# Kernel optimization log

Hardware: AMD Instinct MI355X
Metric: run time of the kernel (lower is better)

## Reference

```python
import jax, jax.numpy as jnp
import numpy as np

N_NODES = 8192   # = in_feats (module ties n_nodes to linear width)
D_FEAT = 512
N_EDGES = 262144  # avg degree 32


def setup_inputs() -> dict:
    key = jax.random.key(0)
    k1, k2, k3 = jax.random.split(key, 3)
    x = jax.random.normal(k1, (D_FEAT, N_NODES), dtype=jnp.float32)
    adj = jax.random.randint(k2, (2, N_EDGES), 0, N_NODES, dtype=jnp.int32)
    # nn.Linear(in_feats, in_feats, bias=False) weight, kaiming-ish scale
    W = jax.random.normal(k3, (N_NODES, N_NODES), dtype=jnp.float32) * (1.0 / np.sqrt(N_NODES))
    return {"x": x, "adj": adj, "W": W}


def reference(x, adj, W):
    # x: [D, N]; adj: [2, E] (row, col); W: [N, N]
    row, col = adj[0], adj[1]
    n = x.shape[1]
    # deg = bincount(row, minlength=N).clamp(min=1)
    deg = jax.ops.segment_sum(jnp.ones_like(row, dtype=x.dtype), row, num_segments=n)
    deg = jnp.maximum(deg, 1.0)
    # spmm(A, ones, N, N, x.T): agg[r] += x.T[c] for each edge (r, c) -> [N, D]
    agg = jax.ops.segment_sum(x.T[col], row, num_segments=n)
    h = agg.T / deg  # [D, N], divide each column by its degree
    # F.relu(self.lin(h)) with Linear applied on last dim (size N = in_feats)
    return jax.nn.relu(h @ W.T)
```

## Files before the change

### kernel.cpp

```cpp
#include <hip/hip_runtime.h>
#include <hip/hip_bf16.h>
#include <stdint.h>

#define NN 8192
#define DD 512
#define EE 262144

typedef __attribute__((ext_vector_type(8))) short short8;
typedef __attribute__((ext_vector_type(4))) float f32x4;

__device__ __forceinline__ unsigned short f2bf_rne(float f) {
    unsigned u = __float_as_uint(f);
    u += 0x7fffu + ((u >> 16) & 1u);
    return (unsigned short)(u >> 16);
}

__device__ __forceinline__ void gload_lds16(const void* g, void* l) {
    __builtin_amdgcn_global_load_lds(
        (const __attribute__((address_space(1))) unsigned int*)g,
        (__attribute__((address_space(3))) unsigned int*)l, 16, 0, 0);
}

__global__ void k_init(int* deg, int* cursor) {
    int i = blockIdx.x * 256 + threadIdx.x;
    if (i < NN) { deg[i] = 0; cursor[i] = 0; }
}

__global__ void k_hist(const int* __restrict__ row, int* __restrict__ deg) {
    int e = blockIdx.x * 256 + threadIdx.x;
    if (e < EE) atomicAdd(&deg[row[e]], 1);
}

__global__ void k_scan(const int* __restrict__ deg, int* __restrict__ offsets,
                       int* __restrict__ cursor) {
    __shared__ int psum[256];
    int t = threadIdx.x;
    int base = t * 32;
    int local[32];
    int s = 0;
    for (int i = 0; i < 32; i++) { local[i] = s; s += deg[base + i]; }
    psum[t] = s;
    __syncthreads();
    int pre = 0;
    for (int i = 0; i < t; i++) pre += psum[i];
    for (int i = 0; i < 32; i++) {
        int v = pre + local[i];
        offsets[base + i] = v;
        cursor[base + i] = v;
    }
    if (t == 255) offsets[NN] = pre + s;
}

__global__ void k_scatter(const int* __restrict__ row, const int* __restrict__ col,
                          int* __restrict__ cursor, int* __restrict__ csr) {
    int e = blockIdx.x * 256 + threadIdx.x;
    if (e < EE) {
        int r = row[e];
        int p = atomicAdd(&cursor[r], 1);
        csr[p] = col[e];
    }
}

__global__ void k_xt(const float* __restrict__ x, unsigned short* __restrict__ xTb) {
    __shared__ float tile[32][33];
    int tx = threadIdx.x & 31, ty = threadIdx.x >> 5;
    int n0 = blockIdx.x * 32;
    int d0 = blockIdx.y * 32;
    #pragma unroll
    for (int i = 0; i < 32; i += 8)
        tile[ty + i][tx] = x[(size_t)(d0 + ty + i) * NN + n0 + tx];
    __syncthreads();
    #pragma unroll
    for (int i = 0; i < 32; i += 8)
        xTb[(size_t)(n0 + ty + i) * DD + d0 + tx] = f2bf_rne(tile[tx][ty + i]);
}

__global__ void k_agg(const unsigned short* __restrict__ xTb, const int* __restrict__ offsets,
                      const int* __restrict__ csr, unsigned short* __restrict__ hTb) {
    __shared__ int nb[128];
    int r = blockIdx.x;
    int t = threadIdx.x;
    int s = offsets[r], e = offsets[r + 1];
    int d = e - s;
    float inv = 1.0f / (float)(d > 0 ? d : 1);
    float a0 = 0.f, a1 = 0.f, a2 = 0.f, a3 = 0.f;
    for (int base = s; base < e; base += 128) {
        int cnt = min(128, e - base);
        if (t < cnt) nb[t] = csr[base + t];
        __syncthreads();
        for (int j = 0; j < cnt; j++) {
            int c = nb[j];
            uint2 u = *(const uint2*)(xTb + (size_t)c * DD + t * 4);
            a0 += __uint_as_float(u.x << 16);
            a1 += __uint_as_float(u.x & 0xffff0000u);
            a2 += __uint_as_float(u.y << 16);
            a3 += __uint_as_float(u.y & 0xffff0000u);
        }
        __syncthreads();
    }
    unsigned short o0 = f2bf_rne(a0 * inv), o1 = f2bf_rne(a1 * inv);
    unsigned short o2 = f2bf_rne(a2 * inv), o3 = f2bf_rne(a3 * inv);
    ushort4 o = make_ushort4(o0, o1, o2, o3);
    *(ushort4*)(hTb + (size_t)r * DD + t * 4) = o;
}

__global__ void k_ht(const unsigned short* __restrict__ hTb, unsigned short* __restrict__ hA) {
    __shared__ unsigned short tile[32][33];
    int tx = threadIdx.x & 31, ty = threadIdx.x >> 5;
    int r0 = blockIdx.x * 32;
    int d0 = blockIdx.y * 32;
    #pragma unroll
    for (int i = 0; i < 32; i += 8)
        tile[ty + i][tx] = hTb[(size_t)(r0 + ty + i) * DD + d0 + tx];
    __syncthreads();
    #pragma unroll
    for (int i = 0; i < 32; i += 8)
        hA[(size_t)(d0 + ty + i) * NN + r0 + tx] = tile[tx][ty + i];
}

__global__ void k_zero(float4* part) {
    int i = blockIdx.x * 256 + threadIdx.x;
    part[i] = make_float4(0.f, 0.f, 0.f, 0.f);
}

__global__ __launch_bounds__(256, 2)
void k_gemm(const unsigned short* __restrict__ hA, const float* __restrict__ W,
            float* __restrict__ part) {
    __shared__ unsigned short As[128 * 64];
    __shared__ unsigned short Bs[128 * 72];

    const int bid = blockIdx.x;
    const int g = (bid & 7) | ((bid >> 5) << 3);
    const int mt = (bid >> 3) & 3;
    const int nt = g >> 1;
    const int ks = g & 1;
    const int m0 = mt * 128, n0 = nt * 128;
    const int kbeg = ks * 4096, kend = kbeg + 4096;

    const int tid = threadIdx.x;
    const int lane = tid & 63, wave = tid >> 6;
    const int wm = (wave & 1) * 64, wn = (wave >> 1) * 64;
    const int l15 = lane & 15, quad = lane >> 4;

    f32x4 acc[4][4];
    #pragma unroll
    for (int i = 0; i < 4; i++)
        #pragma unroll
        for (int j = 0; j < 4; j++) acc[i][j] = (f32x4){0.f, 0.f, 0.f, 0.f};

    const int arow = tid >> 3;
    const int acol_log = ((tid & 7) ^ (arow & 7)) * 8;
    const int aphys = (tid & 7) * 8;

    for (int k0 = kbeg; k0 < kend; k0 += 64) {
        __syncthreads();
        #pragma unroll
        for (int i = 0; i < 4; i++) {
            int r = arow + i * 32;
            gload_lds16(hA + (size_t)(m0 + r) * NN + k0 + acol_log, &As[r * 64 + aphys]);
        }
        float4 wv[8];
        #pragma unroll
        for (int i = 0; i < 8; i++) {
            int fid = tid + i * 256;
            int rw = fid >> 4, c4 = fid & 15;
            wv[i] = *(const float4*)(W + (size_t)(n0 + rw) * NN + k0 + c4 * 4);
        }
        #pragma unroll
        for (int i = 0; i < 8; i++) {
            int fid = tid + i * 256;
            int rw = fid >> 4, c4 = fid & 15;
            unsigned p0 = __builtin_amdgcn_perm(__float_as_uint(wv[i].y) + 0x8000u,
                                                __float_as_uint(wv[i].x) + 0x8000u, 0x07060302u);
            unsigned p1 = __builtin_amdgcn_perm(__float_as_uint(wv[i].w) + 0x8000u,
                                                __float_as_uint(wv[i].z) + 0x8000u, 0x07060302u);
            *(uint2*)&Bs[rw * 72 + c4 * 4] = make_uint2(p0, p1);
        }
        __syncthreads();
        #pragma unroll
        for (int kk = 0; kk < 64; kk += 32) {
            short8 af[4], bf[4];
            #pragma unroll
            for (int mi = 0; mi < 4; mi++) {
                int row = wm + mi * 16 + l15;
                int pc = (((kk >> 3) + quad) ^ (l15 & 7)) * 8;
                af[mi] = *(const short8*)&As[row * 64 + pc];
            }
            #pragma unroll
            for (int ni = 0; ni < 4; ni++)
                bf[ni] = *(const short8*)&Bs[(wn + ni * 16 + l15) * 72 + kk + quad * 8];
            #pragma unroll
            for (int mi = 0; mi < 4; mi++)
                #pragma unroll
                for (int ni = 0; ni < 4; ni++)
                    acc[mi][ni] = __builtin_amdgcn_mfma_f32_16x16x32_bf16(
                        af[mi], bf[ni], acc[mi][ni], 0, 0, 0);
        }
    }
    #pragma unroll
    for (int mi = 0; mi < 4; mi++)
        #pragma unroll
        for (int ni = 0; ni < 4; ni++) {
            int mrow = m0 + wm + mi * 16 + quad * 4;
            int ncol = n0 + wn + ni * 16 + l15;
            #pragma unroll
            for (int i = 0; i < 4; i++)
                atomicAdd(&part[(size_t)(mrow + i) * NN + ncol], acc[mi][ni][i]);
        }
}

__global__ void k_relu(float4* __restrict__ buf) {
    int i = blockIdx.x * 256 + threadIdx.x;
    float4 v = buf[i];
    buf[i] = make_float4(fmaxf(v.x, 0.f), fmaxf(v.y, 0.f), fmaxf(v.z, 0.f), fmaxf(v.w, 0.f));
}

extern "C" void kernel_launch(void* const* d_in, const int* in_sizes, int n_in,
                              void* d_out, int out_size, void* d_ws, size_t ws_size,
                              hipStream_t stream) {
    const float* x = (const float*)d_in[0];
    const int* adj = (const int*)d_in[1];
    const float* W = (const float*)d_in[2];
    char* ws = (char*)d_ws;

    const int* row = adj;
    const int* col = adj + EE;

    int* deg = (int*)(ws + 0);
    int* cursor = (int*)(ws + 32768);
    int* offsets = (int*)(ws + 65536);
    int* csr = (int*)(ws + 131072);
    unsigned short* xTb = (unsigned short*)(ws + (2u << 20));
    unsigned short* hA = xTb;
    unsigned short* hTb = (unsigned short*)d_out;
    float* part = (float*)d_out;

    k_init<<<32, 256, 0, stream>>>(deg, cursor);
    k_hist<<<EE / 256, 256, 0, stream>>>(row, deg);
    k_scan<<<1, 256, 0, stream>>>(deg, offsets, cursor);
    k_scatter<<<EE / 256, 256, 0, stream>>>(row, col, cursor, csr);
    k_xt<<<dim3(NN / 32, DD / 32), 256, 0, stream>>>(x, xTb);
    k_agg<<<NN, 128, 0, stream>>>(xTb, offsets, csr, hTb);
    k_ht<<<dim3(NN / 32, DD / 32), 256, 0, stream>>>(hTb, hA);
    k_zero<<<4096, 256, 0, stream>>>((float4*)part);
    k_gemm<<<512, 256, 0, stream>>>(hA, W, part);
    k_relu<<<4096, 256, 0, stream>>>((float4*)part);
}
```

Baseline: 523.4 us.

## Drop LDS staging in GEMM; load MFMA fragments directly with register double-buffering

The GEMM kernel no longer stages A and W tiles through shared memory with barriers. Each wave now loads its MFMA operand fragments straight from global memory into registers, using two register buffers so the next k-step's loads are in flight while the current MFMA batch runs. W is converted to bf16 in registers just before use. This removes LDS traffic and __syncthreads stalls, but loses data reuse across waves: each A and W row is fetched by two waves, and the direct global access pattern is less coalesced, with more register pressure.

```diff
diff --git a/kernel.cpp b/kernel.cpp
--- a/kernel.cpp
+++ b/kernel.cpp
@@ -13,12 +13,6 @@
     unsigned u = __float_as_uint(f);
     u += 0x7fffu + ((u >> 16) & 1u);
     return (unsigned short)(u >> 16);
-}
-
-__device__ __forceinline__ void gload_lds16(const void* g, void* l) {
-    __builtin_amdgcn_global_load_lds(
-        (const __attribute__((address_space(1))) unsigned int*)g,
-        (__attribute__((address_space(3))) unsigned int*)l, 16, 0, 0);
 }
 
 __global__ void k_init(int* deg, int* cursor) {
@@ -123,15 +117,55 @@
     part[i] = make_float4(0.f, 0.f, 0.f, 0.f);
 }
 
+struct afrag { short8 v[4]; };
+struct wfrag { float4 v[4][2]; };
+
+__device__ __forceinline__ void load_a(afrag& f, const unsigned short* aptr, int k) {
+    #pragma unroll
+    for (int mi = 0; mi < 4; mi++)
+        f.v[mi] = *(const short8*)(aptr + (size_t)mi * 16 * NN + k);
+}
+__device__ __forceinline__ void load_w(wfrag& f, const float* wptr, int k) {
+    #pragma unroll
+    for (int ni = 0; ni < 4; ni++) {
+        f.v[ni][0] = *(const float4*)(wptr + (size_t)ni * 16 * NN + k);
+        f.v[ni][1] = *(const float4*)(wptr + (size_t)ni * 16 * NN + k + 4);
+    }
+}
+__device__ __forceinline__ short8 pack_bf16(const float4& a, const float4& b) {
+    unsigned p0 = __builtin_amdgcn_perm(__float_as_uint(a.y) + 0x8000u,
+                                        __float_as_uint(a.x) + 0x8000u, 0x07060302u);
+    unsigned p1 = __builtin_amdgcn_perm(__float_as_uint(a.w) + 0x8000u,
+                                        __float_as_uint(a.z) + 0x8000u, 0x07060302u);
+    unsigned p2 = __builtin_amdgcn_perm(__float_as_uint(b.y) + 0x8000u,
+                                        __float_as_uint(b.x) + 0x8000u, 0x07060302u);
+    unsigned p3 = __builtin_amdgcn_perm(__float_as_uint(b.w) + 0x8000u,
+                                        __float_as_uint(b.z) + 0x8000u, 0x07060302u);
+    union { unsigned u[4]; short8 s; } r;
+    r.u[0] = p0; r.u[1] = p1; r.u[2] = p2; r.u[3] = p3;
+    return r.s;
+}
+__device__ __forceinline__ void compute(f32x4 acc[4][4], const afrag& a, const wfrag& w) {
+    short8 bf[4];
+    #pragma unroll
+    for (int ni = 0; ni < 4; ni++) bf[ni] = pack_bf16(w.v[ni][0], w.v[ni][1]);
+    #pragma unroll
+    for (int mi = 0; mi < 4; mi++)
+        #pragma unroll
+        for (int ni = 0; ni < 4; ni++)
+            acc[mi][ni] = __builtin_amdgcn_mfma_f32_16x16x32_bf16(
+                a.v[mi], bf[ni], acc[mi][ni], 0, 0, 0);
+}
+
 __global__ __launch_bounds__(256, 2)
 void k_gemm(const unsigned short* __restrict__ hA, const float* __restrict__ W,
             float* __restrict__ part) {
-    __shared__ unsigned short As[128 * 64];
-    __shared__ unsigned short Bs[128 * 72];
-
     const int bid = blockIdx.x;
-    const int g = (bid & 7) | ((bid >> 5) << 3);
-    const int mt = (bid >> 3) & 3;
+    const int x = bid & 7;
+    const int l = bid >> 3;
+    const int mt = l & 3;
+    const int ghi = l >> 2;
+    const int g = ghi * 8 + x;
     const int nt = g >> 1;
     const int ks = g & 1;
     const int m0 = mt * 128, n0 = nt * 128;
@@ -142,61 +176,29 @@
     const int wm = (wave & 1) * 64, wn = (wave >> 1) * 64;
     const int l15 = lane & 15, quad = lane >> 4;
 
+    const unsigned short* aptr = hA + (size_t)(m0 + wm + l15) * NN + quad * 8;
+    const float* wptr = W + (size_t)(n0 + wn + l15) * NN + quad * 8;
+
     f32x4 acc[4][4];
     #pragma unroll
     for (int i = 0; i < 4; i++)
         #pragma unroll
         for (int j = 0; j < 4; j++) acc[i][j] = (f32x4){0.f, 0.f, 0.f, 0.f};
 
-    const int arow = tid >> 3;
-    const int acol_log = ((tid & 7) ^ (arow & 7)) * 8;
-    const int aphys = (tid & 7) * 8;
+    afrag aA, aB;
+    wfrag wA, wB;
+    load_a(aA, aptr, kbeg);      load_w(wA, wptr, kbeg);
+    load_a(aB, aptr, kbeg + 32); load_w(wB, wptr, kbeg + 32);
 
     for (int k0 = kbeg; k0 < kend; k0 += 64) {
-        __syncthreads();
-        #pragma unroll
-        for (int i = 0; i < 4; i++) {
-            int r = arow + i * 32;
-            gload_lds16(hA + (size_t)(m0 + r) * NN + k0 + acol_log, &As[r * 64 + aphys]);
-        }
-        float4 wv[8];
-        #pragma unroll
-        for (int i = 0; i < 8; i++) {
-            int fid = tid + i * 256;
-            int rw = fid >> 4, c4 = fid & 15;
-            wv[i] = *(const float4*)(W + (size_t)(n0 + rw) * NN + k0 + c4 * 4);
-        }
-        #pragma unroll
-        for (int i = 0; i < 8; i++) {
-            int fid = tid + i * 256;
-            int rw = fid >> 4, c4 = fid & 15;
-            unsigned p0 = __builtin_amdgcn_perm(__float_as_uint(wv[i].y) + 0x8000u,
-                                                __float_as_uint(wv[i].x) + 0x8000u, 0x07060302u);
-            unsigned p1 = __builtin_amdgcn_perm(__float_as_uint(wv[i].w) + 0x8000u,
-                                                __float_as_uint(wv[i].z) + 0x8000u, 0x07060302u);
-            *(uint2*)&Bs[rw * 72 + c4 * 4] = make_uint2(p0, p1);
-        }
-        __syncthreads();
-        #pragma unroll
-        for (int kk = 0; kk < 64; kk += 32) {
-            short8 af[4], bf[4];
-            #pragma unroll
-            for (int mi = 0; mi < 4; mi++) {
-                int row = wm + mi * 16 + l15;
-                int pc = (((kk >> 3) + quad) ^ (l15 & 7)) * 8;
-                af[mi] = *(const short8*)&As[row * 64 + pc];
-            }
-            #pragma unroll
-            for (int ni = 0; ni < 4; ni++)
-                bf[ni] = *(const short8*)&Bs[(wn + ni * 16 + l15) * 72 + kk + quad * 8];
-            #pragma unroll
-            for (int mi = 0; mi < 4; mi++)
-                #pragma unroll
-                for (int ni = 0; ni < 4; ni++)
-                    acc[mi][ni] = __builtin_amdgcn_mfma_f32_16x16x32_bf16(
-                        af[mi], bf[ni], acc[mi][ni], 0, 0, 0);
-        }
-    }
+        int kpA = (k0 + 64 < kend) ? k0 + 64 : kbeg;
+        int kpB = (k0 + 96 < kend) ? k0 + 96 : kbeg;
+        compute(acc, aA, wA);
+        load_a(aA, aptr, kpA); load_w(wA, wptr, kpA);
+        compute(acc, aB, wB);
+        load_a(aB, aptr, kpB); load_w(wB, wptr, kpB);
+    }
+
     #pragma unroll
     for (int mi = 0; mi < 4; mi++)
         #pragma unroll
```

Measured after the change: 895.4 us. +71.1%, slower.

## Double-buffer GEMM LDS tiles to overlap next-tile loads with MFMA

Applied to the files above, without the earlier changes.

Splits the A and B shared-memory tiles into two buffers and prefetches the next K-slice while MFMAs run on the current one. W is loaded into registers before compute and converted to bf16 into the other buffer afterwards, and A goes straight to LDS asynchronously. This hides global load latency behind compute and removes one barrier per iteration. In exchange it doubles LDS use, to about 68KB per block, which could limit the two-blocks-per-CU occupancy target, and it holds the prefetched W values in registers across the MFMA section.

```diff
diff --git a/kernel.cpp b/kernel.cpp
--- a/kernel.cpp
+++ b/kernel.cpp
@@ -126,8 +126,8 @@
 __global__ __launch_bounds__(256, 2)
 void k_gemm(const unsigned short* __restrict__ hA, const float* __restrict__ W,
             float* __restrict__ part) {
-    __shared__ unsigned short As[128 * 64];
-    __shared__ unsigned short Bs[128 * 72];
+    __shared__ unsigned short As[2][128 * 64];
+    __shared__ unsigned short Bs[2][128 * 72];
 
     const int bid = blockIdx.x;
     const int g = (bid & 7) | ((bid >> 5) << 3);
@@ -151,32 +151,45 @@
     const int arow = tid >> 3;
     const int acol_log = ((tid & 7) ^ (arow & 7)) * 8;
     const int aphys = (tid & 7) * 8;
-
+    const int brow = tid >> 4;
+    const int bc4 = tid & 15;
+
+    float4 wv[8];
+
+    #pragma unroll
+    for (int i = 0; i < 8; i++)
+        wv[i] = *(const float4*)(W + (size_t)(n0 + brow + i * 16) * NN + kbeg + bc4 * 4);
+    #pragma unroll
+    for (int i = 0; i < 4; i++) {
+        int r = arow + i * 32;
+        gload_lds16(hA + (size_t)(m0 + r) * NN + kbeg + acol_log, &As[0][r * 64 + aphys]);
+    }
+    #pragma unroll
+    for (int i = 0; i < 8; i++) {
+        unsigned p0 = __builtin_amdgcn_perm(__float_as_uint(wv[i].y) + 0x8000u,
+                                            __float_as_uint(wv[i].x) + 0x8000u, 0x07060302u);
+        unsigned p1 = __builtin_amdgcn_perm(__float_as_uint(wv[i].w) + 0x8000u,
+                                            __float_as_uint(wv[i].z) + 0x8000u, 0x07060302u);
+        *(uint2*)&Bs[0][(brow + i * 16) * 72 + bc4 * 4] = make_uint2(p0, p1);
+    }
+    __syncthreads();
+
+    int cur = 0;
     for (int k0 = kbeg; k0 < kend; k0 += 64) {
-        __syncthreads();
-        #pragma unroll
-        for (int i = 0; i < 4; i++) {
-            int r = arow + i * 32;
-            gload_lds16(hA + (size_t)(m0 + r) * NN + k0 + acol_log, &As[r * 64 + aphys]);
-        }
-        float4 wv[8];
-        #pragma unroll
-        for (int i = 0; i < 8; i++) {
-            int fid = tid + i * 256;
-            int rw = fid >> 4, c4 = fid & 15;
-            wv[i] = *(const float4*)(W + (size_t)(n0 + rw) * NN + k0 + c4 * 4);
-        }
-        #pragma unroll
-        for (int i = 0; i < 8; i++) {
-            int fid = tid + i * 256;
-            int rw = fid >> 4, c4 = fid & 15;
-            unsigned p0 = __builtin_amdgcn_perm(__float_as_uint(wv[i].y) + 0x8000u,
-                                                __float_as_uint(wv[i].x) + 0x8000u, 0x07060302u);
-            unsigned p1 = __builtin_amdgcn_perm(__float_as_uint(wv[i].w) + 0x8000u,
-                                                __float_as_uint(wv[i].z) + 0x8000u, 0x07060302u);
-            *(uint2*)&Bs[rw * 72 + c4 * 4] = make_uint2(p0, p1);
-        }
-        __syncthreads();
+        const bool has_next = (k0 + 64 < kend);
+        if (has_next) {
+            #pragma unroll
+            for (int i = 0; i < 8; i++)
+                wv[i] = *(const float4*)(W + (size_t)(n0 + brow + i * 16) * NN +
+                                         (k0 + 64) + bc4 * 4);
+            #pragma unroll
+            for (int i = 0; i < 4; i++) {
+                int r = arow + i * 32;
+                gload_lds16(hA + (size_t)(m0 + r) * NN + (k0 + 64) + acol_log,
+                            &As[cur ^ 1][r * 64 + aphys]);
+            }
+            __builtin_amdgcn_sched_barrier(0);
+        }
         #pragma unroll
         for (int kk = 0; kk < 64; kk += 32) {
             short8 af[4], bf[4];
@@ -184,11 +197,11 @@
             for (int mi = 0; mi < 4; mi++) {
                 int row = wm + mi * 16 + l15;
                 int pc = (((kk >> 3) + quad) ^ (l15 & 7)) * 8;
-                af[mi] = *(const short8*)&As[row * 64 + pc];
+                af[mi] = *(const short8*)&As[cur][row * 64 + pc];
             }
             #pragma unroll
             for (int ni = 0; ni < 4; ni++)
-                bf[ni] = *(const short8*)&Bs[(wn + ni * 16 + l15) * 72 + kk + quad * 8];
+                bf[ni] = *(const short8*)&Bs[cur][(wn + ni * 16 + l15) * 72 + kk + quad * 8];
             #pragma unroll
             for (int mi = 0; mi < 4; mi++)
                 #pragma unroll
@@ -196,7 +209,20 @@
                     acc[mi][ni] = __builtin_amdgcn_mfma_f32_16x16x32_bf16(
                         af[mi], bf[ni], acc[mi][ni], 0, 0, 0);
         }
-    }
+        if (has_next) {
+            #pragma unroll
+            for (int i = 0; i < 8; i++) {
+                unsigned p0 = __builtin_amdgcn_perm(__float_as_uint(wv[i].y) + 0x8000u,
+                                                    __float_as_uint(wv[i].x) + 0x8000u, 0x07060302u);
+                unsigned p1 = __builtin_amdgcn_perm(__float_as_uint(wv[i].w) + 0x8000u,
+                                                    __float_as_uint(wv[i].z) + 0x8000u, 0x07060302u);
+                *(uint2*)&Bs[cur ^ 1][(brow + i * 16) * 72 + bc4 * 4] = make_uint2(p0, p1);
+            }
+        }
+        __syncthreads();
+        cur ^= 1;
+    }
+
     #pragma unroll
     for (int mi = 0; mi < 4; mi++)
         #pragma unroll
```

Result: no change. 527.8 us (+0.8%).
